# Optimization experiments

Measured on AMD Instinct MI355X. Metric: run time of the kernel, lower is better.

## Reference

```python
import jax, jax.numpy as jnp
import numpy as np

SUBSTEPS = 4  # fixed dopri5 substeps per output interval (fixed-step surrogate for adaptive dopri5)
T_TOTAL = 10.0  # torch.linspace(0, 10, T)


def setup_inputs() -> dict:
    key = jax.random.key(0)
    ks = jax.random.split(key, 8)
    B, D, H, T = 1024, 256, 512, 11
    x0 = jax.random.normal(ks[0], (B, 1, D), dtype=jnp.float32)
    # net[0], net[2] weights ~ N(0, 0.01); net[4] and biases: torch default uniform(-1/sqrt(fan_in), 1/sqrt(fan_in))
    W1 = 0.01 * jax.random.normal(ks[1], (H, D), dtype=jnp.float32)
    b1 = jax.random.uniform(ks[2], (H,), minval=-1.0, maxval=1.0, dtype=jnp.float32) / np.float32(np.sqrt(D))
    W2 = 0.01 * jax.random.normal(ks[3], (H, H), dtype=jnp.float32)
    b2 = jax.random.uniform(ks[4], (H,), minval=-1.0, maxval=1.0, dtype=jnp.float32) / np.float32(np.sqrt(H))
    W3 = jax.random.uniform(ks[5], (D, H), minval=-1.0, maxval=1.0, dtype=jnp.float32) / np.float32(np.sqrt(H))
    b3 = jax.random.uniform(ks[6], (D,), minval=-1.0, maxval=1.0, dtype=jnp.float32) / np.float32(np.sqrt(H))
    return {"x0": x0, "T": T, "W1": W1, "b1": b1, "W2": W2, "b2": b2, "W3": W3, "b3": b3}


def _mlp(y, W1, b1, W2, b2, W3, b3):
    h = jax.nn.relu(jnp.dot(y, W1.T) + b1)
    h = jax.nn.relu(jnp.dot(h, W2.T) + b2)
    return jnp.dot(h, W3.T) + b3


def _ode_solve(y0, T, W1, b1, W2, b2, W3, b3):
    # Dopri5 tableau (autonomous dynamics, FSAL stage k7 unused for the 5th-order solution)
    h = np.float32((T_TOTAL / (T - 1)) / SUBSTEPS)

    def f(y):
        return _mlp(y, W1, b1, W2, b2, W3, b3)

    def rk_step(y, _):
        k1 = f(y)
        k2 = f(y + h * (1.0 / 5.0) * k1)
        k3 = f(y + h * (3.0 / 40.0 * k1 + 9.0 / 40.0 * k2))
        k4 = f(y + h * (44.0 / 45.0 * k1 - 56.0 / 15.0 * k2 + 32.0 / 9.0 * k3))
        k5 = f(y + h * (19372.0 / 6561.0 * k1 - 25360.0 / 2187.0 * k2
                        + 64448.0 / 6561.0 * k3 - 212.0 / 729.0 * k4))
        k6 = f(y + h * (9017.0 / 3168.0 * k1 - 355.0 / 33.0 * k2 + 46732.0 / 5247.0 * k3
                        + 49.0 / 176.0 * k4 - 5103.0 / 18656.0 * k5))
        y_next = y + h * (35.0 / 384.0 * k1 + 500.0 / 1113.0 * k3 + 125.0 / 192.0 * k4
                          - 2187.0 / 6784.0 * k5 + 11.0 / 84.0 * k6)
        return y_next, None

    def interval(y, _):
        y, _ = jax.lax.scan(rk_step, y, None, length=SUBSTEPS)
        return y, y

    _, ys = jax.lax.scan(interval, y0, None, length=T - 1)  # [T-1, B, D]
    return ys


def reference(x0, T, W1, b1, W2, b2, W3, b3):
    y0 = x0[:, 0, :]  # squeeze(1)
    ys = _ode_solve(y0, T, W1, b1, W2, b2, W3, b3)  # [T-1, B, D] (time points 1..T-1)
    pred = jnp.transpose(ys, (1, 0, 2))  # [B, T-1, D] == permute(1,0,2) then [:, 1:]
    return pred
```

## Files before the change

kernel.cpp:

```cpp
#include <hip/hip_runtime.h>
#include <hip/hip_bf16.h>
#include <stdint.h>
#include <stddef.h>


typedef __bf16 bf16x8 __attribute__((ext_vector_type(8)));
typedef __bf16 bf16x4 __attribute__((ext_vector_type(4)));
typedef float  f32x4  __attribute__((ext_vector_type(4)));

#define DD 256
#define HH 512
#define RA 264
#define RH 520

#define W1P_OFF 0
#define W2P_OFF 131072
#define W3P_OFF (131072+262144)

__global__ void cvt_w(const float* __restrict__ W1, const float* __restrict__ W2,
                      const float* __restrict__ W3, __bf16* __restrict__ o)
{
    int i = blockIdx.x * blockDim.x + threadIdx.x;
    const float* src;
    __bf16* dst;
    if (i < 16384) {
        int c = i, lane = c & 63, kb = (c >> 6) & 7, t = c >> 9;
        src = W1 + (size_t)(t*16 + (lane & 15))*DD + kb*32 + (lane >> 4)*8;
        dst = o + W1P_OFF + (size_t)c*8;
    } else if (i < 49152) {
        int c = i - 16384, lane = c & 63, kb = (c >> 6) & 15, t = c >> 10;
        src = W2 + (size_t)(t*16 + (lane & 15))*HH + kb*32 + (lane >> 4)*8;
        dst = o + W2P_OFF + (size_t)c*8;
    } else {
        int c = i - 49152, lane = c & 63, kb = (c >> 6) & 15, t = c >> 10;
        src = W3 + (size_t)(t*16 + (lane & 15))*HH + kb*32 + (lane >> 4)*8;
        dst = o + W3P_OFF + (size_t)c*8;
    }
#pragma unroll
    for (int e = 0; e < 8; ++e) dst[e] = (__bf16)src[e];
}

__device__ __forceinline__ void wg_barrier() {
    asm volatile("s_waitcnt lgkmcnt(0)" ::: "memory");
    __builtin_amdgcn_s_barrier();
    asm volatile("" ::: "memory");
}

__global__ __launch_bounds__(1024) __attribute__((amdgpu_waves_per_eu(4, 4)))
void ode_kernel(const float* __restrict__ x0, const int* __restrict__ Tp,
                const __bf16* __restrict__ Wp,
                const float* __restrict__ b1, const float* __restrict__ b2,
                const float* __restrict__ b3, float* __restrict__ out)
{
    __shared__ __bf16 sA [16 * RA];
    __shared__ __bf16 sH1[16 * RH];
    __shared__ __bf16 sH2[16 * RH];
    __shared__ float  sb1[HH], sb2[HH], sb3[DD];

    const int   nT = *Tp - 1;
    const float hs = 10.0f / (float)nT * 0.25f;

    const int tid  = threadIdx.x;
    const int w    = tid >> 6;
    const int lane = tid & 63;
    const int lr   = lane & 15;
    const int lg   = lane >> 4;
    const int brow = blockIdx.x * 16 + lr;

    const __bf16* wp1 = Wp + W1P_OFF + (size_t)w * 8192  + lane * 8;
    const __bf16* wp2 = Wp + W2P_OFF + (size_t)w * 16384 + lane * 8;
    const __bf16* wp3 = Wp + W3P_OFF + (size_t)w * 8192  + lane * 8;

    if (tid < HH) { sb1[tid] = b1[tid]; sb2[tid] = b2[tid]; }
    if (tid < DD) { sb3[tid] = b3[tid]; }

    f32x4 yy = *(const f32x4*)(x0 + (size_t)brow * DD + w*16 + lg*4);
    f32x4 k1, k2, k3, k4, k5, k6;

    __bf16*       sAw  = sA  + lr*RA + w*16 + lg*4;
    __bf16*       sH1w = sH1 + lr*RH + w*32 + lg*4;
    __bf16*       sH2w = sH2 + lr*RH + w*32 + lg*4;
    const __bf16* apA  = sA  + lr*RA + lg*8;
    const __bf16* apH1 = sH1 + lr*RH + lg*8;
    const __bf16* apH2 = sH2 + lr*RH + lg*8;

    auto store_stage = [&](f32x4 v) {
        bf16x4 o;
#pragma unroll
        for (int j = 0; j < 4; ++j) o[j] = (__bf16)v[j];
        *(bf16x4*)sAw = o;
    };

    auto mlp = [&](f32x4& kout) {
        wg_barrier();
        f32x4 a0 = *(const f32x4*)(sb1 + w*32 + lg*4);
        f32x4 a1 = *(const f32x4*)(sb1 + w*32 + 16 + lg*4);
#pragma unroll
        for (int kb = 0; kb < 8; ++kb) {
            bf16x8 b   = *(const bf16x8*)(apA + kb*32);
            bf16x8 wa0 = *(const bf16x8*)(wp1 + kb*512);
            bf16x8 wa1 = *(const bf16x8*)(wp1 + 4096 + kb*512);
            a0 = __builtin_amdgcn_mfma_f32_16x16x32_bf16(wa0, b, a0, 0, 0, 0);
            a1 = __builtin_amdgcn_mfma_f32_16x16x32_bf16(wa1, b, a1, 0, 0, 0);
        }
        {
            bf16x4 v0, v1;
#pragma unroll
            for (int j = 0; j < 4; ++j) {
                v0[j] = (__bf16)fmaxf(a0[j], 0.0f);
                v1[j] = (__bf16)fmaxf(a1[j], 0.0f);
            }
            *(bf16x4*)sH1w        = v0;
            *(bf16x4*)(sH1w + 16) = v1;
        }
        wg_barrier();
        a0 = *(const f32x4*)(sb2 + w*32 + lg*4);
        a1 = *(const f32x4*)(sb2 + w*32 + 16 + lg*4);
#pragma unroll
        for (int kb = 0; kb < 16; ++kb) {
            bf16x8 b   = *(const bf16x8*)(apH1 + kb*32);
            bf16x8 wa0 = *(const bf16x8*)(wp2 + kb*512);
            bf16x8 wa1 = *(const bf16x8*)(wp2 + 8192 + kb*512);
            a0 = __builtin_amdgcn_mfma_f32_16x16x32_bf16(wa0, b, a0, 0, 0, 0);
            a1 = __builtin_amdgcn_mfma_f32_16x16x32_bf16(wa1, b, a1, 0, 0, 0);
        }
        {
            bf16x4 v0, v1;
#pragma unroll
            for (int j = 0; j < 4; ++j) {
                v0[j] = (__bf16)fmaxf(a0[j], 0.0f);
                v1[j] = (__bf16)fmaxf(a1[j], 0.0f);
            }
            *(bf16x4*)sH2w        = v0;
            *(bf16x4*)(sH2w + 16) = v1;
        }
        wg_barrier();
        f32x4 a = *(const f32x4*)(sb3 + w*16 + lg*4);
#pragma unroll
        for (int kb = 0; kb < 16; ++kb) {
            bf16x8 b  = *(const bf16x8*)(apH2 + kb*32);
            bf16x8 wa = *(const bf16x8*)(wp3 + kb*512);
            a = __builtin_amdgcn_mfma_f32_16x16x32_bf16(wa, b, a, 0, 0, 0);
        }
        kout = a;
    };

    for (int t = 0; t < nT; ++t) {
        for (int ss = 0; ss < 4; ++ss) {
            store_stage(yy);
            mlp(k1);

            store_stage(yy + hs * (0.2f * k1));
            mlp(k2);

            store_stage(yy + hs * ((3.0f/40.0f)*k1 + (9.0f/40.0f)*k2));
            mlp(k3);

            store_stage(yy + hs * ((float)(44.0/45.0)*k1 - (float)(56.0/15.0)*k2
                                  + (float)(32.0/9.0)*k3));
            mlp(k4);

            store_stage(yy + hs * ((float)(19372.0/6561.0)*k1 - (float)(25360.0/2187.0)*k2
                                  + (float)(64448.0/6561.0)*k3 - (float)(212.0/729.0)*k4));
            mlp(k5);

            store_stage(yy + hs * ((float)(9017.0/3168.0)*k1 - (float)(355.0/33.0)*k2
                                  + (float)(46732.0/5247.0)*k3 + (float)(49.0/176.0)*k4
                                  - (float)(5103.0/18656.0)*k5));
            mlp(k6);

            yy = yy + hs * ((float)(35.0/384.0)*k1 + (float)(500.0/1113.0)*k3
                           + (float)(125.0/192.0)*k4 + (float)(-2187.0/6784.0)*k5
                           + (float)(11.0/84.0)*k6);
        }
        *(f32x4*)(out + ((size_t)brow * nT + t) * DD + w*16 + lg*4) = yy;
    }
}

extern "C" void kernel_launch(void* const* d_in, const int* in_sizes, int n_in,
                              void* d_out, int out_size, void* d_ws, size_t ws_size,
                              hipStream_t stream)
{
    const float* x0 = (const float*)d_in[0];
    const int*   Tp = (const int*)  d_in[1];
    const float* W1 = (const float*)d_in[2];
    const float* b1 = (const float*)d_in[3];
    const float* W2 = (const float*)d_in[4];
    const float* b2 = (const float*)d_in[5];
    const float* W3 = (const float*)d_in[6];
    const float* b3 = (const float*)d_in[7];

    const int B = in_sizes[0] / DD;

    __bf16* wb = (__bf16*)d_ws;
    cvt_w<<<256, 256, 0, stream>>>(W1, W2, W3, wb);

    ode_kernel<<<B / 16, 1024, 0, stream>>>(x0, Tp, wb, b1, b2, b3, (float*)d_out);
}
```

Before: 2.866 ms.

## Pin early weight fragments in registers/LDS and software-pipeline remaining weight loads

The head of each layer's bf16 weight fragments is kept resident for the whole kernel: ten fragments in VGPRs and six more per wave in a new LDS buffer. The remaining fragments stream from global memory through a 6-deep rotating register queue that prefetches across layer boundaries, wrapping from layer 3 back to layer 1. This hides global/L2 load latency behind the MFMA chain instead of issuing loads and MFMAs back-to-back. The cost is higher VGPR pressure under a fixed waves_per_eu(4,4) bound, which risks spills, plus roughly 96KB of extra LDS per block.

```diff
diff --git a/kernel.cpp b/kernel.cpp
--- a/kernel.cpp
+++ b/kernel.cpp
@@ -7,6 +7,7 @@
 typedef __bf16 bf16x8 __attribute__((ext_vector_type(8)));
 typedef __bf16 bf16x4 __attribute__((ext_vector_type(4)));
 typedef float  f32x4  __attribute__((ext_vector_type(4)));
+typedef int    i32x4  __attribute__((ext_vector_type(4)));
 
 #define DD 256
 #define HH 512
@@ -16,6 +17,9 @@
 #define W1P_OFF 0
 #define W2P_OFF 131072
 #define W3P_OFF (131072+262144)
+
+#define MFMA(A,B,C) __builtin_amdgcn_mfma_f32_16x16x32_bf16((A),(B),(C),0,0,0)
+#define BC(X) __builtin_bit_cast(bf16x8, (X))
 
 __global__ void cvt_w(const float* __restrict__ W1, const float* __restrict__ W2,
                       const float* __restrict__ W3, __bf16* __restrict__ o)
@@ -55,6 +59,7 @@
     __shared__ __bf16 sA [16 * RA];
     __shared__ __bf16 sH1[16 * RH];
     __shared__ __bf16 sH2[16 * RH];
+    __shared__ __bf16 lwcs[16 * 6 * 512];
     __shared__ float  sb1[HH], sb2[HH], sb3[DD];
 
     const int   nT = *Tp - 1;
@@ -67,12 +72,43 @@
     const int lg   = lane >> 4;
     const int brow = blockIdx.x * 16 + lr;
 
-    const __bf16* wp1 = Wp + W1P_OFF + (size_t)w * 8192  + lane * 8;
-    const __bf16* wp2 = Wp + W2P_OFF + (size_t)w * 16384 + lane * 8;
-    const __bf16* wp3 = Wp + W3P_OFF + (size_t)w * 8192  + lane * 8;
+    const int o1 = w * 8192;
+    const int o2 = W2P_OFF + w * 16384;
+    const int o3 = W3P_OFF + w * 8192;
+    const __bf16* wpl = Wp + lane * 8;
+
+    i32x4 pw0 = *(const i32x4*)(wpl + o1);
+    i32x4 pw1 = *(const i32x4*)(wpl + o1 + 4096);
+    i32x4 pw2 = *(const i32x4*)(wpl + o2);
+    i32x4 pw3 = *(const i32x4*)(wpl + o2 + 8192);
+    i32x4 pw4 = *(const i32x4*)(wpl + o2 + 512);
+    i32x4 pw5 = *(const i32x4*)(wpl + o2 + 8192 + 512);
+    i32x4 pw6 = *(const i32x4*)(wpl + o3);
+    i32x4 pw7 = *(const i32x4*)(wpl + o3 + 512);
+    i32x4 pw8 = *(const i32x4*)(wpl + o3 + 1024);
+    i32x4 pw9 = *(const i32x4*)(wpl + o3 + 1536);
+    asm volatile("" : "+v"(pw0), "+v"(pw1), "+v"(pw2), "+v"(pw3), "+v"(pw4));
+    asm volatile("" : "+v"(pw5), "+v"(pw6), "+v"(pw7), "+v"(pw8), "+v"(pw9));
+
+    {
+        const int coff[6] = { o1 + 512, o1 + 4096 + 512,
+                              o2 + 1024, o2 + 8192 + 1024,
+                              o3 + 2048, o3 + 2560 };
+#pragma unroll
+        for (int c = 0; c < 6; ++c) {
+            i32x4 v = *(const i32x4*)(wpl + coff[c]);
+            *(i32x4*)(lwcs + (w*6 + c)*512 + lane*8) = v;
+        }
+    }
+    const __bf16* lwc = lwcs + w * 6 * 512 + lane * 8;
 
     if (tid < HH) { sb1[tid] = b1[tid]; sb2[tid] = b2[tid]; }
     if (tid < DD) { sb3[tid] = b3[tid]; }
+
+    i32x4 wq[6];
+#pragma unroll
+    for (int j = 0; j < 6; ++j)
+        wq[j] = *(const i32x4*)(wpl + o1 + (j & 1)*4096 + (2 + j/2)*512);
 
     f32x4 yy = *(const f32x4*)(x0 + (size_t)brow * DD + w*16 + lg*4);
     f32x4 k1, k2, k3, k4, k5, k6;
@@ -95,13 +131,25 @@
         wg_barrier();
         f32x4 a0 = *(const f32x4*)(sb1 + w*32 + lg*4);
         f32x4 a1 = *(const f32x4*)(sb1 + w*32 + 16 + lg*4);
-#pragma unroll
-        for (int kb = 0; kb < 8; ++kb) {
-            bf16x8 b   = *(const bf16x8*)(apA + kb*32);
-            bf16x8 wa0 = *(const bf16x8*)(wp1 + kb*512);
-            bf16x8 wa1 = *(const bf16x8*)(wp1 + 4096 + kb*512);
-            a0 = __builtin_amdgcn_mfma_f32_16x16x32_bf16(wa0, b, a0, 0, 0, 0);
-            a1 = __builtin_amdgcn_mfma_f32_16x16x32_bf16(wa1, b, a1, 0, 0, 0);
+        {
+            bf16x8 b = *(const bf16x8*)(apA + 0*32);
+            a0 = MFMA(BC(pw0), b, a0);
+            a1 = MFMA(BC(pw1), b, a1);
+            b = *(const bf16x8*)(apA + 1*32);
+            a0 = MFMA(*(const bf16x8*)(lwc + 0*512), b, a0);
+            a1 = MFMA(*(const bf16x8*)(lwc + 1*512), b, a1);
+        }
+#pragma unroll
+        for (int j = 0; j < 12; ++j) {
+            const int kb = 2 + j/2;
+            bf16x8 b  = *(const bf16x8*)(apA + kb*32);
+            bf16x8 wa = BC(wq[j % 6]);
+            const int nj = j + 6;
+            const int noff = (nj < 12)
+                ? (o1 + (nj & 1)*4096 + (2 + nj/2)*512)
+                : (o2 + ((nj-12) & 1)*8192 + (3 + (nj-12)/2)*512);
+            wq[j % 6] = *(const i32x4*)(wpl + noff);
+            if ((j & 1) == 0) a0 = MFMA(wa, b, a0); else a1 = MFMA(wa, b, a1);
         }
         {
             bf16x4 v0, v1;
@@ -116,13 +164,27 @@
         wg_barrier();
         a0 = *(const f32x4*)(sb2 + w*32 + lg*4);
         a1 = *(const f32x4*)(sb2 + w*32 + 16 + lg*4);
-#pragma unroll
-        for (int kb = 0; kb < 16; ++kb) {
-            bf16x8 b   = *(const bf16x8*)(apH1 + kb*32);
-            bf16x8 wa0 = *(const bf16x8*)(wp2 + kb*512);
-            bf16x8 wa1 = *(const bf16x8*)(wp2 + 8192 + kb*512);
-            a0 = __builtin_amdgcn_mfma_f32_16x16x32_bf16(wa0, b, a0, 0, 0, 0);
-            a1 = __builtin_amdgcn_mfma_f32_16x16x32_bf16(wa1, b, a1, 0, 0, 0);
+        {
+            bf16x8 b = *(const bf16x8*)(apH1 + 0*32);
+            a0 = MFMA(BC(pw2), b, a0);
+            a1 = MFMA(BC(pw3), b, a1);
+            b = *(const bf16x8*)(apH1 + 1*32);
+            a0 = MFMA(BC(pw4), b, a0);
+            a1 = MFMA(BC(pw5), b, a1);
+            b = *(const bf16x8*)(apH1 + 2*32);
+            a0 = MFMA(*(const bf16x8*)(lwc + 2*512), b, a0);
+            a1 = MFMA(*(const bf16x8*)(lwc + 3*512), b, a1);
+        }
+#pragma unroll
+        for (int j = 0; j < 26; ++j) {
+            const int kb = 3 + j/2;
+            bf16x8 b  = *(const bf16x8*)(apH1 + kb*32);
+            bf16x8 wa = BC(wq[j % 6]);
+            const int noff = (j < 20)
+                ? (o2 + ((j+6) & 1)*8192 + (3 + (j+6)/2)*512)
+                : (o3 + (6 + (j-20))*512);
+            wq[j % 6] = *(const i32x4*)(wpl + noff);
+            if ((j & 1) == 0) a0 = MFMA(wa, b, a0); else a1 = MFMA(wa, b, a1);
         }
         {
             bf16x4 v0, v1;
@@ -136,11 +198,30 @@
         }
         wg_barrier();
         f32x4 a = *(const f32x4*)(sb3 + w*16 + lg*4);
-#pragma unroll
-        for (int kb = 0; kb < 16; ++kb) {
+        {
+            bf16x8 b = *(const bf16x8*)(apH2 + 0*32);
+            a = MFMA(BC(pw6), b, a);
+            b = *(const bf16x8*)(apH2 + 1*32);
+            a = MFMA(BC(pw7), b, a);
+            b = *(const bf16x8*)(apH2 + 2*32);
+            a = MFMA(BC(pw8), b, a);
+            b = *(const bf16x8*)(apH2 + 3*32);
+            a = MFMA(BC(pw9), b, a);
+            b = *(const bf16x8*)(apH2 + 4*32);
+            a = MFMA(*(const bf16x8*)(lwc + 4*512), b, a);
+            b = *(const bf16x8*)(apH2 + 5*32);
+            a = MFMA(*(const bf16x8*)(lwc + 5*512), b, a);
+        }
+#pragma unroll
+        for (int j = 0; j < 10; ++j) {
+            const int kb = 6 + j;
             bf16x8 b  = *(const bf16x8*)(apH2 + kb*32);
-            bf16x8 wa = *(const bf16x8*)(wp3 + kb*512);
-            a = __builtin_amdgcn_mfma_f32_16x16x32_bf16(wa, b, a, 0, 0, 0);
+            bf16x8 wa = BC(wq[(2 + j) % 6]);
+            const int noff = (j < 4)
+                ? (o3 + (12 + j)*512)
+                : (o1 + ((j-4) & 1)*4096 + (2 + (j-4)/2)*512);
+            wq[(2 + j) % 6] = *(const i32x4*)(wpl + noff);
+            a = MFMA(wa, b, a);
         }
         kout = a;
     };
```

Measured after the change: 4.863 ms. 69.7% more time.

## Stream MLP weights through per-wave LDS ring via async global_load_lds prefetch

Applied to the files above, without the earlier changes.

Each wave now DMAs its packed bf16 weight chunks into a 4-slot LDS ring with global_load_lds, issued four chunks ahead, instead of loading weights straight from global memory into registers. The prefetch index runs continuously across layers and MLP calls, so the first chunks of the next evaluation are already in flight. Explicit vmcnt and lgkmcnt waits order the DMA against the LDS reads. The goal is to hide L2 latency on weight fetches and free registers. In exchange it adds 64KB of LDS, a shallow fixed prefetch depth, and a full lgkmcnt drain on every k-step, which could serialize the loop.

```diff
diff --git a/kernel.cpp b/kernel.cpp
--- a/kernel.cpp
+++ b/kernel.cpp
@@ -16,6 +16,10 @@
 #define W1P_OFF 0
 #define W2P_OFF 131072
 #define W3P_OFF (131072+262144)
+
+#define MFMA(A,B,C) __builtin_amdgcn_mfma_f32_16x16x32_bf16((A),(B),(C),0,0,0)
+#define VMWAIT(N) asm volatile("s_waitcnt vmcnt(" #N ")" ::: "memory")
+#define LGKM0()   asm volatile("s_waitcnt lgkmcnt(0)" ::: "memory")
 
 __global__ void cvt_w(const float* __restrict__ W1, const float* __restrict__ W2,
                       const float* __restrict__ W3, __bf16* __restrict__ o)
@@ -46,6 +50,19 @@
     asm volatile("" ::: "memory");
 }
 
+typedef __attribute__((address_space(3))) uint32_t       lds_u32;
+typedef const __attribute__((address_space(1))) uint32_t g_u32;
+__device__ __forceinline__ void dma16(const __bf16* g, __bf16* l) {
+    __builtin_amdgcn_global_load_lds((g_u32*)(uintptr_t)g,
+                                     (lds_u32*)(uint32_t)(uintptr_t)l, 16, 0, 0);
+}
+
+__device__ __forceinline__ int chunk_off(int w, int c) {
+    if (c < 16) return w*8192 + (c&1)*4096 + (c>>1)*512;
+    if (c < 48) return W2P_OFF + w*16384 + ((c-16)&1)*8192 + ((c-16)>>1)*512;
+    return W3P_OFF + w*8192 + (c-48)*512;
+}
+
 __global__ __launch_bounds__(1024) __attribute__((amdgpu_waves_per_eu(4, 4)))
 void ode_kernel(const float* __restrict__ x0, const int* __restrict__ Tp,
                 const __bf16* __restrict__ Wp,
@@ -55,6 +72,7 @@
     __shared__ __bf16 sA [16 * RA];
     __shared__ __bf16 sH1[16 * RH];
     __shared__ __bf16 sH2[16 * RH];
+    __shared__ __bf16 stage[16 * 4 * 512];
     __shared__ float  sb1[HH], sb2[HH], sb3[DD];
 
     const int   nT = *Tp - 1;
@@ -67,9 +85,13 @@
     const int lg   = lane >> 4;
     const int brow = blockIdx.x * 16 + lr;
 
-    const __bf16* wp1 = Wp + W1P_OFF + (size_t)w * 8192  + lane * 8;
-    const __bf16* wp2 = Wp + W2P_OFF + (size_t)w * 16384 + lane * 8;
-    const __bf16* wp3 = Wp + W3P_OFF + (size_t)w * 8192  + lane * 8;
+    const __bf16* wpl  = Wp + lane * 8;
+    __bf16*       ring = stage + w * 4 * 512;
+    const __bf16* rgl  = ring + lane * 8;
+
+    auto dma = [&](int c) {
+        dma16(wpl + chunk_off(w, c & 63), ring + (c & 3) * 512);
+    };
 
     if (tid < HH) { sb1[tid] = b1[tid]; sb2[tid] = b2[tid]; }
     if (tid < DD) { sb3[tid] = b3[tid]; }
@@ -84,6 +106,8 @@
     const __bf16* apH1 = sH1 + lr*RH + lg*8;
     const __bf16* apH2 = sH2 + lr*RH + lg*8;
 
+    dma(0); dma(1); dma(2); dma(3);
+
     auto store_stage = [&](f32x4 v) {
         bf16x4 o;
 #pragma unroll
@@ -97,11 +121,15 @@
         f32x4 a1 = *(const f32x4*)(sb1 + w*32 + 16 + lg*4);
 #pragma unroll
         for (int kb = 0; kb < 8; ++kb) {
+            const int c0 = 2*kb;
+            VMWAIT(2);
             bf16x8 b   = *(const bf16x8*)(apA + kb*32);
-            bf16x8 wa0 = *(const bf16x8*)(wp1 + kb*512);
-            bf16x8 wa1 = *(const bf16x8*)(wp1 + 4096 + kb*512);
-            a0 = __builtin_amdgcn_mfma_f32_16x16x32_bf16(wa0, b, a0, 0, 0, 0);
-            a1 = __builtin_amdgcn_mfma_f32_16x16x32_bf16(wa1, b, a1, 0, 0, 0);
+            bf16x8 wa0 = *(const bf16x8*)(rgl + ((c0    ) & 3)*512);
+            bf16x8 wa1 = *(const bf16x8*)(rgl + ((c0 + 1) & 3)*512);
+            a0 = MFMA(wa0, b, a0);
+            a1 = MFMA(wa1, b, a1);
+            LGKM0();
+            dma(c0 + 4); dma(c0 + 5);
         }
         {
             bf16x4 v0, v1;
@@ -118,11 +146,15 @@
         a1 = *(const f32x4*)(sb2 + w*32 + 16 + lg*4);
 #pragma unroll
         for (int kb = 0; kb < 16; ++kb) {
+            const int c0 = 16 + 2*kb;
+            VMWAIT(2);
             bf16x8 b   = *(const bf16x8*)(apH1 + kb*32);
-            bf16x8 wa0 = *(const bf16x8*)(wp2 + kb*512);
-            bf16x8 wa1 = *(const bf16x8*)(wp2 + 8192 + kb*512);
-            a0 = __builtin_amdgcn_mfma_f32_16x16x32_bf16(wa0, b, a0, 0, 0, 0);
-            a1 = __builtin_amdgcn_mfma_f32_16x16x32_bf16(wa1, b, a1, 0, 0, 0);
+            bf16x8 wa0 = *(const bf16x8*)(rgl + ((c0    ) & 3)*512);
+            bf16x8 wa1 = *(const bf16x8*)(rgl + ((c0 + 1) & 3)*512);
+            a0 = MFMA(wa0, b, a0);
+            a1 = MFMA(wa1, b, a1);
+            LGKM0();
+            dma(c0 + 4); dma(c0 + 5);
         }
         {
             bf16x4 v0, v1;
@@ -138,9 +170,13 @@
         f32x4 a = *(const f32x4*)(sb3 + w*16 + lg*4);
 #pragma unroll
         for (int kb = 0; kb < 16; ++kb) {
+            const int c = 48 + kb;
+            VMWAIT(3);
             bf16x8 b  = *(const bf16x8*)(apH2 + kb*32);
-            bf16x8 wa = *(const bf16x8*)(wp3 + kb*512);
-            a = __builtin_amdgcn_mfma_f32_16x16x32_bf16(wa, b, a, 0, 0, 0);
+            bf16x8 wa = *(const bf16x8*)(rgl + (c & 3)*512);
+            a = MFMA(wa, b, a);
+            LGKM0();
+            dma(c + 4);
         }
         kout = a;
     };
@@ -175,6 +211,7 @@
         }
         *(f32x4*)(out + ((size_t)brow * nT + t) * DD + w*16 + lg*4) = yy;
     }
+    VMWAIT(0);
 }
 
 extern "C" void kernel_launch(void* const* d_in, const int* in_sizes, int n_in,
```

New measurement: 4.003 ms. +39.7%, slower.
